# Optimization experiments

Hardware: AMD Instinct MI355X
Metric: run time of the kernel (lower is better)

Reference implementation:

```python
import jax, jax.numpy as jnp
import numpy as np

N = 50000
E = 800000
IN = 128
H = 256


def _sage_conv(x, src, dst, W_l, b_l, W_r, n_nodes):
    # PyG SAGEConv (aggr='mean'): out = lin_l(mean_{j in N(i)} x_j) + lin_r(x_i)
    msg = x[src]                                             # [E, d] gather
    agg = jax.ops.segment_sum(msg, dst, num_segments=n_nodes)  # [N, d]
    cnt = jax.ops.segment_sum(jnp.ones((src.shape[0],), x.dtype), dst,
                              num_segments=n_nodes)
    agg = agg / jnp.maximum(cnt, 1.0)[:, None]               # scatter-mean
    return agg @ W_l + b_l + x @ W_r


def setup_inputs() -> dict:
    key = jax.random.key(0)
    ks = jax.random.split(key, 12)
    s_in, s_h, s_h2 = 1.0 / np.sqrt(IN), 1.0 / np.sqrt(H), 1.0 / np.sqrt(H // 2)
    return {
        "x": jax.random.normal(ks[0], (N, IN), jnp.float32),
        "edge_index": jax.random.randint(ks[1], (2, E), 0, N, dtype=jnp.int32),
        # conv1: in -> H
        "W1_l": jax.random.uniform(ks[2], (IN, H), jnp.float32, -s_in, s_in),
        "b1_l": jnp.zeros((H,), jnp.float32),
        "W1_r": jax.random.uniform(ks[3], (IN, H), jnp.float32, -s_in, s_in),
        # conv2: H -> H
        "W2_l": jax.random.uniform(ks[4], (H, H), jnp.float32, -s_h, s_h),
        "b2_l": jnp.zeros((H,), jnp.float32),
        "W2_r": jax.random.uniform(ks[5], (H, H), jnp.float32, -s_h, s_h),
        # risk head: H -> H//2 -> 1
        "Wh1": jax.random.uniform(ks[6], (H, H // 2), jnp.float32, -s_h, s_h),
        "bh1": jax.random.uniform(ks[7], (H // 2,), jnp.float32, -s_h, s_h),
        "Wh2": jax.random.uniform(ks[8], (H // 2, 1), jnp.float32, -s_h2, s_h2),
        "bh2": jax.random.uniform(ks[9], (1,), jnp.float32, -s_h2, s_h2),
    }


def reference(x, edge_index, W1_l, b1_l, W1_r, W2_l, b2_l, W2_r,
              Wh1, bh1, Wh2, bh2):
    src, dst = edge_index[0], edge_index[1]
    h = jax.nn.relu(_sage_conv(x, src, dst, W1_l, b1_l, W1_r, N))
    h = jax.nn.relu(_sage_conv(h, src, dst, W2_l, b2_l, W2_r, N))
    # risk head (dropout is identity in inference)
    h = jax.nn.relu(h @ Wh1 + bh1)
    return jax.nn.sigmoid(h @ Wh2 + bh2)            # [N, 1]
```

## Files before the change

### kernel.cpp

```cpp
#include <hip/hip_runtime.h>
#include <cstdint>
#include <cstddef>

#define N_NODES 50000
#define N_PAD 50048
#define N_EDGES 800000
#define DIM_IN 128
#define DIM_H 256
#define CAP 64
#define NBKT 391
#define BCAP 2560
#define BINA_BLOCKS 400
#define EPB 2000

using u16 = unsigned short;
using u32 = unsigned int;
using u8 = unsigned char;

typedef __attribute__((ext_vector_type(8))) short bf16x8;
typedef __attribute__((ext_vector_type(4))) float f32x4;
typedef __attribute__((ext_vector_type(2))) float f32x2;

__device__ __forceinline__ u16 f2bf(float x) {
    u32 u = __float_as_uint(x);
    u32 r = (u + 0x7fffu + ((u >> 16) & 1u)) >> 16;
    return (u16)r;
}

__device__ __forceinline__ u8 enc1_sw(float f) {
    u32 u = __float_as_uint(f);
    u32 s = (u >> 24) & 0x80u;
    u32 a = u & 0x7fffffffu;
    if (a >= 0x43e00000u) return (u8)(s | 0x7e);
    if (a < 0x3c800000u) return (u8)s;
    u32 r = a + 0x7ffffu + ((a >> 20) & 1u);
    u32 e8 = (r >> 23) - 120u;
    if (e8 >= 16u) return (u8)(s | 0x7e);
    return (u8)(s | (e8 << 3) | ((r >> 20) & 7u));
}

__device__ __forceinline__ u32 enc4(float f0, float f1, float f2, float f3) {
#if __has_builtin(__builtin_amdgcn_cvt_pk_fp8_f32)
    int w = __builtin_amdgcn_cvt_pk_fp8_f32(f0, f1, 0, false);
    w = __builtin_amdgcn_cvt_pk_fp8_f32(f2, f3, w, true);
    return (u32)w;
#else
    return (u32)enc1_sw(f0) | ((u32)enc1_sw(f1) << 8) |
           ((u32)enc1_sw(f2) << 16) | ((u32)enc1_sw(f3) << 24);
#endif
}

__device__ __forceinline__ u8 enc1(float f) {
#if __has_builtin(__builtin_amdgcn_cvt_pk_fp8_f32)
    return (u8)(__builtin_amdgcn_cvt_pk_fp8_f32(f, 0.f, 0, false) & 0xff);
#else
    return enc1_sw(f);
#endif
}

__device__ __forceinline__ void dec_u32(float* o, u32 w) {
#if __has_builtin(__builtin_amdgcn_cvt_pk_f32_fp8)
    f32x2 a = __builtin_amdgcn_cvt_pk_f32_fp8(w, false);
    f32x2 b = __builtin_amdgcn_cvt_pk_f32_fp8(w, true);
    o[0] = a[0]; o[1] = a[1]; o[2] = b[0]; o[3] = b[1];
#else
    #pragma unroll
    for (int k = 0; k < 4; ++k) {
        u32 x = (w >> (8 * k)) & 0xffu;
        u32 bits = ((x & 0x80u) << 24) | ((x & 0x7fu) << 20);
        o[k] = __uint_as_float(bits) * __uint_as_float(0x7b800000u);
    }
#endif
}

__device__ __forceinline__ void gld_lds16(const u16* g, u16* l) {
    __builtin_amdgcn_global_load_lds(
        (__attribute__((address_space(1))) void*)g,
        (__attribute__((address_space(3))) void*)l, 16, 0, 0);
}

__global__ __launch_bounds__(256) void binA(
    const int* __restrict__ src, const int* __restrict__ dst,
    int* __restrict__ gcur, int2* __restrict__ binbuf) {
    __shared__ int hist[NBKT];
    __shared__ int base[NBKT];
    const int tid = threadIdx.x;
    const int e0 = blockIdx.x * EPB;
    const int e1 = min(e0 + EPB, N_EDGES);
    for (int t = tid; t < NBKT; t += 256) hist[t] = 0;
    __syncthreads();
    for (int i = e0 + tid; i < e1; i += 256)
        atomicAdd(&hist[dst[i] >> 7], 1);
    __syncthreads();
    for (int t = tid; t < NBKT; t += 256) {
        int h = hist[t];
        base[t] = h ? atomicAdd(&gcur[t], h) : 0;
    }
    __syncthreads();
    for (int t = tid; t < NBKT; t += 256) hist[t] = 0;
    __syncthreads();
    for (int i = e0 + tid; i < e1; i += 256) {
        int d = dst[i];
        int b = d >> 7;
        int o = base[b] + atomicAdd(&hist[b], 1);
        if (o < (b + 1) * BCAP) binbuf[o] = make_int2(src[i], d);
    }
}

__global__ __launch_bounds__(256) void binB(
    const int* __restrict__ gcur, const int2* __restrict__ binbuf,
    int* __restrict__ cnt, int* __restrict__ csr) {
    __shared__ int lcnt[128];
    __shared__ int lcsr[128 * CAP];
    const int b = blockIdx.x;
    const int tid = threadIdx.x;
    if (tid < 128) lcnt[tid] = 0;
    __syncthreads();
    int gc = gcur[b] - b * BCAP;
    if (gc > BCAP) gc = BCAP;
    for (int i = tid; i < gc; i += 256) {
        int2 p = binbuf[b * BCAP + i];
        int n = p.y & 127;
        int slot = atomicAdd(&lcnt[n], 1);
        if (slot < CAP) lcsr[n * CAP + slot] = p.x;
    }
    __syncthreads();
    const uint4* ls = reinterpret_cast<const uint4*>(lcsr);
    uint4* gs = reinterpret_cast<uint4*>(csr + (size_t)b * 128 * CAP);
    for (int i = tid; i < 128 * CAP / 4; i += 256) gs[i] = ls[i];
    if (tid < 128) {
        int v = b * 128 + tid;
        if (v < N_NODES) cnt[v] = lcnt[tid];
    }
}

__global__ __launch_bounds__(256) void prep(
    const float* __restrict__ x,
    const float* __restrict__ W1_l, const float* __restrict__ W1_r,
    const float* __restrict__ W2_l, const float* __restrict__ W2_r,
    const float* __restrict__ Wh1,
    u16* __restrict__ x_hi, u32* __restrict__ x_f8,
    u16* __restrict__ w1l, u16* __restrict__ w1r,
    u16* __restrict__ w2l, u16* __restrict__ w2r, u16* __restrict__ wh1,
    int* __restrict__ gcur) {
    int b = blockIdx.x, tid = threadIdx.x;
    if (b < 2) {
        int i = b * 256 + tid;
        if (i < NBKT) gcur[i] = i * BCAP;
        return;
    }
    b -= 2;
    if (b < 6250) {
        int i = b * 256 + tid;
        float4 v = reinterpret_cast<const float4*>(x)[i];
        ushort4 h;
        h.x = f2bf(v.x); h.y = f2bf(v.y); h.z = f2bf(v.z); h.w = f2bf(v.w);
        reinterpret_cast<ushort4*>(x_hi)[i] = h;
        x_f8[i] = enc4(v.x, v.y, v.z, v.w);
        return;
    }
    b -= 6250;
    if (b < 128) {
        int idx = b * 256 + tid; int m = idx >> 7, k = idx & 127;
        w1l[idx] = f2bf(W1_l[(size_t)k * 256 + m]); return;
    }
    b -= 128;
    if (b < 128) {
        int idx = b * 256 + tid; int m = idx >> 7, k = idx & 127;
        w1r[idx] = f2bf(W1_r[(size_t)k * 256 + m]); return;
    }
    b -= 128;
    if (b < 256) {
        int idx = b * 256 + tid; int m = idx >> 8, k = idx & 255;
        w2l[idx] = f2bf(W2_l[(size_t)k * 256 + m]); return;
    }
    b -= 256;
    if (b < 256) {
        int idx = b * 256 + tid; int m = idx >> 8, k = idx & 255;
        w2r[idx] = f2bf(W2_r[(size_t)k * 256 + m]); return;
    }
    b -= 256;
    {
        int idx = b * 256 + tid; int m = idx >> 8, k = idx & 255;
        wh1[idx] = f2bf(Wh1[(size_t)k * 128 + m]);
    }
}

__device__ __forceinline__ void acc16_add(float* acc, uint4 a) {
    float t[4];
    dec_u32(t, a.x); acc[0] += t[0]; acc[1] += t[1]; acc[2] += t[2]; acc[3] += t[3];
    dec_u32(t, a.y); acc[4] += t[0]; acc[5] += t[1]; acc[6] += t[2]; acc[7] += t[3];
    dec_u32(t, a.z); acc[8] += t[0]; acc[9] += t[1]; acc[10] += t[2]; acc[11] += t[3];
    dec_u32(t, a.w); acc[12] += t[0]; acc[13] += t[1]; acc[14] += t[2]; acc[15] += t[3];
}

template <int U4ROW>
__global__ __launch_bounds__(256) void aggregate_f8(
    const uint4* __restrict__ tab, const int* __restrict__ cnt,
    const int* __restrict__ csr, u16* __restrict__ out_hi, int n_nodes) {
    constexpr int EPI = 64 / U4ROW;
    constexpr int D = U4ROW * 16;
    const int lane = threadIdx.x & 63;
    const int v = blockIdx.x * 4 + (threadIdx.x >> 6);
    if (v >= n_nodes) return;
    const int q = lane & (U4ROW - 1);
    const int e = lane / U4ROW;
    const int d = cnt[v];
    const int dl = min(d, CAP);
    const int myidx = (lane < dl) ? csr[v * CAP + lane] : 0;
    float acc[16] = {};
    int j = 0;
    for (; j + 2 * EPI <= dl; j += 2 * EPI) {
        int i0 = __shfl(myidx, j + e, 64);
        int i1 = __shfl(myidx, j + EPI + e, 64);
        uint4 a = tab[(size_t)i0 * U4ROW + q];
        uint4 b = tab[(size_t)i1 * U4ROW + q];
        acc16_add(acc, a);
        acc16_add(acc, b);
    }
    for (; j + EPI <= dl; j += EPI) {
        int i0 = __shfl(myidx, j + e, 64);
        uint4 a = tab[(size_t)i0 * U4ROW + q];
        acc16_add(acc, a);
    }
    int r = dl - j;
    if (r > 0) {
        int ee = (e < r) ? e : 0;
        int i0 = __shfl(myidx, j + ee, 64);
        uint4 a = tab[(size_t)i0 * U4ROW + q];
        if (e < r) acc16_add(acc, a);
    }
    #pragma unroll
    for (int s = U4ROW; s < 64; s <<= 1)
        #pragma unroll
        for (int i = 0; i < 16; ++i) acc[i] += __shfl_xor(acc[i], s, 64);
    const float inv = 1.f / (float)((d > 0) ? d : 1);
    if (e == 0) {
        u32 w[8];
        #pragma unroll
        for (int k = 0; k < 8; ++k) {
            float m0 = acc[2 * k] * inv, m1 = acc[2 * k + 1] * inv;
            w[k] = ((u32)f2bf(m1) << 16) | f2bf(m0);
        }
        u16* dp = out_hi + (size_t)v * D + q * 16;
        *reinterpret_cast<uint4*>(dp) = *reinterpret_cast<uint4*>(&w[0]);
        *reinterpret_cast<uint4*>(dp + 8) = *reinterpret_cast<uint4*>(&w[4]);
    }
}

template <int MODE>
__global__ __launch_bounds__(512) void gemm_fused(
    const u16* __restrict__ Ah1, const u16* __restrict__ Ah2,
    const u16* __restrict__ Bh1, const u16* __restrict__ Bh2,
    const float* __restrict__ bias,
    const u16* __restrict__ wh1t, const float* __restrict__ bh1,
    const float* __restrict__ wh2, const float* __restrict__ bh2,
    u16* __restrict__ Chi, u8* __restrict__ Cf8, float* __restrict__ outF,
    int nrows, int K) {
    __shared__ u16 SMEM[(MODE == 1) ? 37888 : 12288];
    u16* As = SMEM;
    u16* Bs = SMEM + 4096;

    const int tid = threadIdx.x;
    const int lane = tid & 63;
    const int w = tid >> 6;
    const int wr = w >> 2, wc = w & 3;
    const int row0 = blockIdx.x * 128;

    const u16* const Aph[2] = {Ah1, Ah2};
    const u16* const Bph[2] = {Bh1, Bh2};

    f32x4 zero4 = {0.f, 0.f, 0.f, 0.f};
    f32x4 acc[4][4];
    #pragma unroll
    for (int i = 0; i < 4; ++i)
        #pragma unroll
        for (int j = 0; j < 4; ++j) acc[i][j] = zero4;

    const int srow = lane >> 2;
    const int schunk = (lane & 3) * 8;

    const int nks = K >> 5;
    for (int ph = 0; ph < 2; ++ph) {
        const u16* Ab = Aph[ph];
        const u16* Bb = Bph[ph];
        for (int kk = 0; kk < nks; ++kk) {
            #pragma unroll
            for (int t = 0; t < 3; ++t) {
                int slab = w * 3 + t;
                if (slab < 8) {
                    int grow = row0 + slab * 16 + srow;
                    if (grow > nrows - 1) grow = nrows - 1;
                    gld_lds16(Ab + (size_t)grow * K + kk * 32 + schunk,
                              As + slab * 512);
                } else {
                    int gcol = (slab - 8) * 16 + srow;
                    gld_lds16(Bb + (size_t)gcol * K + kk * 32 + schunk,
                              Bs + (slab - 8) * 512);
                }
            }
            __syncthreads();
            bf16x8 af[4], bfr[4];
            #pragma unroll
            for (int i = 0; i < 4; ++i)
                af[i] = *reinterpret_cast<const bf16x8*>(
                    &As[(wr * 64 + i * 16 + (lane & 15)) * 32 + (lane >> 4) * 8]);
            #pragma unroll
            for (int j = 0; j < 4; ++j)
                bfr[j] = *reinterpret_cast<const bf16x8*>(
                    &Bs[(wc * 64 + j * 16 + (lane & 15)) * 32 + (lane >> 4) * 8]);
            #pragma unroll
            for (int i = 0; i < 4; ++i)
                #pragma unroll
                for (int j = 0; j < 4; ++j)
                    acc[i][j] = __builtin_amdgcn_mfma_f32_16x16x32_bf16(
                        af[i], bfr[j], acc[i][j], 0, 0, 0);
            __syncthreads();
        }
    }

    if (MODE == 0) {
        #pragma unroll
        for (int i = 0; i < 4; ++i) {
            #pragma unroll
            for (int j = 0; j < 4; ++j) {
                int col = wc * 64 + j * 16 + (lane & 15);
                float b = bias[col];
                #pragma unroll
                for (int r = 0; r < 4; ++r) {
                    int row = row0 + wr * 64 + i * 16 + (lane >> 4) * 4 + r;
                    if (row < nrows) {
                        float v = fmaxf(acc[i][j][r] + b, 0.f);
                        Chi[(size_t)row * 256 + col] = f2bf(v);
                        Cf8[(size_t)row * 256 + col] = enc1(v);
                    }
                }
            }
        }
    } else {
        char* hb = (char*)SMEM;
        #pragma unroll
        for (int i = 0; i < 4; ++i)
            #pragma unroll
            for (int j = 0; j < 4; ++j) {
                int col = wc * 64 + j * 16 + (lane & 15);
                float b = bias[col];
                #pragma unroll
                for (int r = 0; r < 4; ++r) {
                    int row = wr * 64 + i * 16 + (lane >> 4) * 4 + r;
                    float v = fmaxf(acc[i][j][r] + b, 0.f);
                    int byt = row * 512 + col * 2;
                    *(u16*)(hb + (byt ^ ((row & 7) << 4))) = f2bf(v);
                }
            }
        __syncthreads();

        u16* Bs2 = SMEM + 32768;
        float* hpart = (float*)(SMEM + 32768 + 4096);
        const int whr = wr, whc = wc;
        f32x4 acc2[4][2];
        #pragma unroll
        for (int i = 0; i < 4; ++i) {
            acc2[i][0] = zero4; acc2[i][1] = zero4;
        }
        for (int kk = 0; kk < 8; ++kk) {
            {
                int gcol = w * 16 + srow;
                gld_lds16(wh1t + (size_t)gcol * 256 + kk * 32 + schunk,
                          Bs2 + w * 512);
            }
            __syncthreads();
            bf16x8 af2[4], bfr2[2];
            #pragma unroll
            for (int i = 0; i < 4; ++i) {
                int row = whr * 64 + i * 16 + (lane & 15);
                int byt = row * 512 + kk * 64 + (lane >> 4) * 16;
                af2[i] = *reinterpret_cast<const bf16x8*>(hb + (byt ^ ((row & 7) << 4)));
            }
            #pragma unroll
            for (int j = 0; j < 2; ++j)
                bfr2[j] = *reinterpret_cast<const bf16x8*>(
                    &Bs2[(whc * 32 + j * 16 + (lane & 15)) * 32 + (lane >> 4) * 8]);
            #pragma unroll
            for (int i = 0; i < 4; ++i)
                #pragma unroll
                for (int j = 0; j < 2; ++j)
                    acc2[i][j] = __builtin_amdgcn_mfma_f32_16x16x32_bf16(
                        af2[i], bfr2[j], acc2[i][j], 0, 0, 0);
            __syncthreads();
        }

        float pr[4][4];
        #pragma unroll
        for (int i = 0; i < 4; ++i)
            #pragma unroll
            for (int r = 0; r < 4; ++r) pr[i][r] = 0.f;
        #pragma unroll
        for (int j = 0; j < 2; ++j) {
            int col = whc * 32 + j * 16 + (lane & 15);
            float b1 = bh1[col];
            float wv = wh2[col];
            #pragma unroll
            for (int i = 0; i < 4; ++i)
                #pragma unroll
                for (int r = 0; r < 4; ++r)
                    pr[i][r] += fmaxf(acc2[i][j][r] + b1, 0.f) * wv;
        }
        #pragma unroll
        for (int i = 0; i < 4; ++i)
            #pragma unroll
            for (int r = 0; r < 4; ++r) {
                float s = pr[i][r];
                s += __shfl_xor(s, 1, 64);
                s += __shfl_xor(s, 2, 64);
                s += __shfl_xor(s, 4, 64);
                s += __shfl_xor(s, 8, 64);
                pr[i][r] = s;
            }
        if ((lane & 15) == 0) {
            #pragma unroll
            for (int i = 0; i < 4; ++i)
                #pragma unroll
                for (int r = 0; r < 4; ++r)
                    hpart[whc * 128 + whr * 64 + i * 16 + (lane >> 4) * 4 + r] = pr[i][r];
        }
        __syncthreads();
        if (tid < 128) {
            int row = row0 + tid;
            if (row < nrows) {
                float s = hpart[tid] + hpart[128 + tid] + hpart[256 + tid]
                        + hpart[384 + tid] + bh2[0];
                outF[row] = 1.f / (1.f + expf(-s));
            }
        }
    }
}

static inline size_t align256(size_t x) { return (x + 255) & ~(size_t)255; }

extern "C" void kernel_launch(void* const* d_in, const int* in_sizes, int n_in,
                              void* d_out, int out_size, void* d_ws, size_t ws_size,
                              hipStream_t stream) {
    const float* x    = (const float*)d_in[0];
    const int* ei     = (const int*)d_in[1];
    const float* W1_l = (const float*)d_in[2];
    const float* b1_l = (const float*)d_in[3];
    const float* W1_r = (const float*)d_in[4];
    const float* W2_l = (const float*)d_in[5];
    const float* b2_l = (const float*)d_in[6];
    const float* W2_r = (const float*)d_in[7];
    const float* Wh1  = (const float*)d_in[8];
    const float* bh1  = (const float*)d_in[9];
    const float* Wh2  = (const float*)d_in[10];
    const float* bh2  = (const float*)d_in[11];
    float* out = (float*)d_out;

    const int* src = ei;
    const int* dst = ei + N_EDGES;

    const size_t SZ_N128 = (size_t)N_NODES * DIM_IN * sizeof(u16);
    const size_t SZ_N256 = (size_t)N_NODES * DIM_H * sizeof(u16);
    const size_t SZ_W128x256 = (size_t)128 * 256 * sizeof(u16);

    char* ws = (char*)d_ws;
    size_t off_ = 0;
    auto alloc = [&](size_t bytes) { size_t o = off_; off_ += align256(bytes); return o; };

    size_t o_cnt = alloc((size_t)N_PAD * 4);
    size_t o_gcur = alloc((size_t)512 * 4);
    size_t o_csr = alloc((size_t)N_PAD * CAP * 4);
    size_t o_bin = alloc((size_t)NBKT * BCAP * 8);
    size_t o_w1l = alloc(SZ_W128x256);
    size_t o_w1r = alloc(SZ_W128x256);
    size_t o_w2l = alloc(2 * SZ_W128x256);
    size_t o_w2r = alloc(2 * SZ_W128x256);
    size_t o_wh1 = alloc(SZ_W128x256);
    size_t o_xh  = alloc(SZ_N128);
    size_t o_xf8 = alloc((size_t)N_NODES * DIM_IN);
    size_t o_a1  = alloc(SZ_N128);
    size_t o_h1  = alloc(SZ_N256);
    size_t o_h1f = alloc((size_t)N_NODES * DIM_H);
    size_t o_a2  = alloc(SZ_N256);
    if (ws_size < off_) return;

    int* cnt  = (int*)(ws + o_cnt);
    int* gcur = (int*)(ws + o_gcur);
    int* csr  = (int*)(ws + o_csr);
    int2* binbuf = (int2*)(ws + o_bin);
    u16* w1l_h = (u16*)(ws + o_w1l);
    u16* w1r_h = (u16*)(ws + o_w1r);
    u16* w2l_h = (u16*)(ws + o_w2l);
    u16* w2r_h = (u16*)(ws + o_w2r);
    u16* wh1_h = (u16*)(ws + o_wh1);
    u16* x_hi    = (u16*)(ws + o_xh);
    u32* x_f8    = (u32*)(ws + o_xf8);
    u16* agg1_hi = (u16*)(ws + o_a1);
    u16* h1_hi   = (u16*)(ws + o_h1);
    u8*  h1_f8   = (u8*)(ws + o_h1f);
    u16* agg2_hi = (u16*)(ws + o_a2);

    prep<<<2 + 6250 + 128 + 128 + 256 + 256 + 128, 256, 0, stream>>>(
        x, W1_l, W1_r, W2_l, W2_r, Wh1,
        x_hi, x_f8, w1l_h, w1r_h, w2l_h, w2r_h, wh1_h, gcur);

    binA<<<BINA_BLOCKS, 256, 0, stream>>>(src, dst, gcur, binbuf);
    binB<<<NBKT, 256, 0, stream>>>(gcur, binbuf, cnt, csr);

    const int RB = (N_NODES + 127) / 128;
    const int AB = (N_NODES + 3) / 4;

    aggregate_f8<8><<<AB, 256, 0, stream>>>(
        (const uint4*)x_f8, cnt, csr, agg1_hi, N_NODES);
    gemm_fused<0><<<RB, 512, 0, stream>>>(
        agg1_hi, x_hi, w1l_h, w1r_h, b1_l,
        nullptr, nullptr, nullptr, nullptr, h1_hi, h1_f8, nullptr, N_NODES, 128);

    aggregate_f8<16><<<AB, 256, 0, stream>>>(
        (const uint4*)h1_f8, cnt, csr, agg2_hi, N_NODES);
    gemm_fused<1><<<RB, 512, 0, stream>>>(
        agg2_hi, h1_hi, w2l_h, w2r_h, b2_l,
        wh1_h, bh1, Wh2, bh2, nullptr, nullptr, out, N_NODES, 256);
}
```

Measured before the change: 153.7 us.

## Double-buffer GEMM LDS tiles, swizzle LDS layout, and stage epilogue stores through LDS

The fused GEMM now double-buffers its A/B tiles in LDS, issuing the global-to-LDS load for the next k-slice before computing on the current one, with a single barrier per iteration instead of two. LDS chunks are XOR-swizzled to avoid bank conflicts on the fragment reads, and the risk-head weight loads get the same double-buffering. The MODE 0 epilogue writes its results to LDS first and then emits coalesced 16-byte global stores, so the h1 buffers are padded to N_PAD rows because the row bound check is dropped. LDS usage roughly doubles, which may lower occupancy.

```diff
diff --git a/kernel.cpp b/kernel.cpp
--- a/kernel.cpp
+++ b/kernel.cpp
@@ -257,9 +257,7 @@
     const float* __restrict__ wh2, const float* __restrict__ bh2,
     u16* __restrict__ Chi, u8* __restrict__ Cf8, float* __restrict__ outF,
     int nrows, int K) {
-    __shared__ u16 SMEM[(MODE == 1) ? 37888 : 12288];
-    u16* As = SMEM;
-    u16* Bs = SMEM + 4096;
+    __shared__ __align__(16) u16 SMEM[(MODE == 1) ? 41984 : 24576];
 
     const int tid = threadIdx.x;
     const int lane = tid & 63;
@@ -267,9 +265,6 @@
     const int wr = w >> 2, wc = w & 3;
     const int row0 = blockIdx.x * 128;
 
-    const u16* const Aph[2] = {Ah1, Ah2};
-    const u16* const Bph[2] = {Bh1, Bh2};
-
     f32x4 zero4 = {0.f, 0.f, 0.f, 0.f};
     f32x4 acc[4][4];
     #pragma unroll
@@ -278,66 +273,102 @@
         for (int j = 0; j < 4; ++j) acc[i][j] = zero4;
 
     const int srow = lane >> 2;
-    const int schunk = (lane & 3) * 8;
+    const int swz = (((lane & 3) ^ (srow & 3)) * 8);
 
     const int nks = K >> 5;
-    for (int ph = 0; ph < 2; ++ph) {
-        const u16* Ab = Aph[ph];
-        const u16* Bb = Bph[ph];
-        for (int kk = 0; kk < nks; ++kk) {
-            #pragma unroll
-            for (int t = 0; t < 3; ++t) {
-                int slab = w * 3 + t;
-                if (slab < 8) {
-                    int grow = row0 + slab * 16 + srow;
-                    if (grow > nrows - 1) grow = nrows - 1;
-                    gld_lds16(Ab + (size_t)grow * K + kk * 32 + schunk,
-                              As + slab * 512);
-                } else {
-                    int gcol = (slab - 8) * 16 + srow;
-                    gld_lds16(Bb + (size_t)gcol * K + kk * 32 + schunk,
-                              Bs + (slab - 8) * 512);
-                }
+    const int NIT = 2 * nks;
+
+    auto stage = [&](int it, int buf) {
+        const int ph = (it >= nks) ? 1 : 0;
+        const int kk = it - ph * nks;
+        const u16* Ab = ph ? Ah2 : Ah1;
+        const u16* Bb = ph ? Bh2 : Bh1;
+        u16* base = SMEM + buf * 12288;
+        #pragma unroll
+        for (int t = 0; t < 3; ++t) {
+            int slab = w * 3 + t;
+            if (slab < 8) {
+                int grow = row0 + slab * 16 + srow;
+                if (grow > nrows - 1) grow = nrows - 1;
+                gld_lds16(Ab + (size_t)grow * K + kk * 32 + swz, base + slab * 512);
+            } else {
+                int gcol = (slab - 8) * 16 + srow;
+                gld_lds16(Bb + (size_t)gcol * K + kk * 32 + swz,
+                          base + 4096 + (slab - 8) * 512);
+            }
+        }
+    };
+
+    stage(0, 0);
+    __syncthreads();
+    int cur = 0;
+    for (int it = 0; it < NIT; ++it) {
+        if (it + 1 < NIT) stage(it + 1, cur ^ 1);
+        const char* As_ = (const char*)(SMEM + cur * 12288);
+        const char* Bs_ = As_ + 8192;
+        bf16x8 af[4], bfr[4];
+        #pragma unroll
+        for (int i = 0; i < 4; ++i) {
+            int tr = wr * 64 + i * 16 + (lane & 15);
+            af[i] = *reinterpret_cast<const bf16x8*>(
+                As_ + tr * 64 + (((lane >> 4) ^ (tr & 3)) * 16));
+        }
+        #pragma unroll
+        for (int j = 0; j < 4; ++j) {
+            int tc = wc * 64 + j * 16 + (lane & 15);
+            bfr[j] = *reinterpret_cast<const bf16x8*>(
+                Bs_ + tc * 64 + (((lane >> 4) ^ (tc & 3)) * 16));
+        }
+        #pragma unroll
+        for (int i = 0; i < 4; ++i)
+            #pragma unroll
+            for (int j = 0; j < 4; ++j)
+                acc[i][j] = __builtin_amdgcn_mfma_f32_16x16x32_bf16(
+                    af[i], bfr[j], acc[i][j], 0, 0, 0);
+        __syncthreads();
+        cur ^= 1;
+    }
+
+    if (MODE == 0) {
+        u16* hL = SMEM;
+        u8* fL = (u8*)SMEM + 32768;
+        #pragma unroll
+        for (int half = 0; half < 2; ++half) {
+            if (wr == half) {
+                #pragma unroll
+                for (int i = 0; i < 4; ++i)
+                    #pragma unroll
+                    for (int j = 0; j < 4; ++j) {
+                        int col = wc * 64 + j * 16 + (lane & 15);
+                        float b = bias[col];
+                        #pragma unroll
+                        for (int r = 0; r < 4; ++r) {
+                            int rl = i * 16 + (lane >> 4) * 4 + r;
+                            float v = fmaxf(acc[i][j][r] + b, 0.f);
+                            hL[rl * 256 + col] = f2bf(v);
+                            fL[rl * 256 + col] = enc1(v);
+                        }
+                    }
             }
             __syncthreads();
-            bf16x8 af[4], bfr[4];
-            #pragma unroll
-            for (int i = 0; i < 4; ++i)
-                af[i] = *reinterpret_cast<const bf16x8*>(
-                    &As[(wr * 64 + i * 16 + (lane & 15)) * 32 + (lane >> 4) * 8]);
-            #pragma unroll
-            for (int j = 0; j < 4; ++j)
-                bfr[j] = *reinterpret_cast<const bf16x8*>(
-                    &Bs[(wc * 64 + j * 16 + (lane & 15)) * 32 + (lane >> 4) * 8]);
-            #pragma unroll
-            for (int i = 0; i < 4; ++i)
-                #pragma unroll
-                for (int j = 0; j < 4; ++j)
-                    acc[i][j] = __builtin_amdgcn_mfma_f32_16x16x32_bf16(
-                        af[i], bfr[j], acc[i][j], 0, 0, 0);
+            size_t gr0 = (size_t)(row0 + half * 64);
+            uint4* gh = reinterpret_cast<uint4*>(Chi + gr0 * 256);
+            const uint4* lh = reinterpret_cast<const uint4*>(hL);
+            #pragma unroll
+            for (int k2 = 0; k2 < 4; ++k2) gh[tid + k2 * 512] = lh[tid + k2 * 512];
+            uint4* gf = reinterpret_cast<uint4*>(Cf8 + gr0 * 256);
+            const uint4* lf = reinterpret_cast<const uint4*>(fL);
+            #pragma unroll
+            for (int k2 = 0; k2 < 2; ++k2) gf[tid + k2 * 512] = lf[tid + k2 * 512];
             __syncthreads();
         }
-    }
-
-    if (MODE == 0) {
-        #pragma unroll
-        for (int i = 0; i < 4; ++i) {
-            #pragma unroll
-            for (int j = 0; j < 4; ++j) {
-                int col = wc * 64 + j * 16 + (lane & 15);
-                float b = bias[col];
-                #pragma unroll
-                for (int r = 0; r < 4; ++r) {
-                    int row = row0 + wr * 64 + i * 16 + (lane >> 4) * 4 + r;
-                    if (row < nrows) {
-                        float v = fmaxf(acc[i][j][r] + b, 0.f);
-                        Chi[(size_t)row * 256 + col] = f2bf(v);
-                        Cf8[(size_t)row * 256 + col] = enc1(v);
-                    }
-                }
-            }
-        }
     } else {
+        u16* Bs2 = SMEM + 32768;
+        float* hpart = (float*)(SMEM + 40960);
+        {
+            int gcol = w * 16 + srow;
+            gld_lds16(wh1t + (size_t)gcol * 256 + 0 * 32 + swz, Bs2 + w * 512);
+        }
         char* hb = (char*)SMEM;
         #pragma unroll
         for (int i = 0; i < 4; ++i)
@@ -355,21 +386,18 @@
             }
         __syncthreads();
 
-        u16* Bs2 = SMEM + 32768;
-        float* hpart = (float*)(SMEM + 32768 + 4096);
         const int whr = wr, whc = wc;
         f32x4 acc2[4][2];
         #pragma unroll
-        for (int i = 0; i < 4; ++i) {
-            acc2[i][0] = zero4; acc2[i][1] = zero4;
-        }
+        for (int i = 0; i < 4; ++i) { acc2[i][0] = zero4; acc2[i][1] = zero4; }
+        int curH = 0;
         for (int kk = 0; kk < 8; ++kk) {
-            {
+            if (kk + 1 < 8) {
                 int gcol = w * 16 + srow;
-                gld_lds16(wh1t + (size_t)gcol * 256 + kk * 32 + schunk,
-                          Bs2 + w * 512);
-            }
-            __syncthreads();
+                gld_lds16(wh1t + (size_t)gcol * 256 + (kk + 1) * 32 + swz,
+                          Bs2 + (curH ^ 1) * 4096 + w * 512);
+            }
+            const char* B2 = (const char*)(Bs2 + curH * 4096);
             bf16x8 af2[4], bfr2[2];
             #pragma unroll
             for (int i = 0; i < 4; ++i) {
@@ -378,9 +406,11 @@
                 af2[i] = *reinterpret_cast<const bf16x8*>(hb + (byt ^ ((row & 7) << 4)));
             }
             #pragma unroll
-            for (int j = 0; j < 2; ++j)
+            for (int j = 0; j < 2; ++j) {
+                int tc = whc * 32 + j * 16 + (lane & 15);
                 bfr2[j] = *reinterpret_cast<const bf16x8*>(
-                    &Bs2[(whc * 32 + j * 16 + (lane & 15)) * 32 + (lane >> 4) * 8]);
+                    B2 + tc * 64 + (((lane >> 4) ^ (tc & 3)) * 16));
+            }
             #pragma unroll
             for (int i = 0; i < 4; ++i)
                 #pragma unroll
@@ -388,6 +418,7 @@
                     acc2[i][j] = __builtin_amdgcn_mfma_f32_16x16x32_bf16(
                         af2[i], bfr2[j], acc2[i][j], 0, 0, 0);
             __syncthreads();
+            curH ^= 1;
         }
 
         float pr[4][4];
@@ -459,7 +490,6 @@
     const int* dst = ei + N_EDGES;
 
     const size_t SZ_N128 = (size_t)N_NODES * DIM_IN * sizeof(u16);
-    const size_t SZ_N256 = (size_t)N_NODES * DIM_H * sizeof(u16);
     const size_t SZ_W128x256 = (size_t)128 * 256 * sizeof(u16);
 
     char* ws = (char*)d_ws;
@@ -478,9 +508,9 @@
     size_t o_xh  = alloc(SZ_N128);
     size_t o_xf8 = alloc((size_t)N_NODES * DIM_IN);
     size_t o_a1  = alloc(SZ_N128);
-    size_t o_h1  = alloc(SZ_N256);
-    size_t o_h1f = alloc((size_t)N_NODES * DIM_H);
-    size_t o_a2  = alloc(SZ_N256);
+    size_t o_h1  = alloc((size_t)N_PAD * DIM_H * sizeof(u16));
+    size_t o_h1f = alloc((size_t)N_PAD * DIM_H);
+    size_t o_a2  = alloc((size_t)N_NODES * DIM_H * sizeof(u16));
     if (ws_size < off_) return;
 
     int* cnt  = (int*)(ws + o_cnt);
```

After: 157.6 us. +2.5%, slower.
